# Kernel tuning notes

Measured on AMD Instinct MI355X. Metric: run time of the kernel, lower is better.

Reference implementation:

```python
import jax, jax.numpy as jnp
import numpy as np

N_NODES = 100000
N_EDGES = 1600000
HIDDEN = 128
N_ETYPES = 4
N_STEPS = 4


def setup_inputs() -> dict:
    key = jax.random.key(0)
    ks = jax.random.split(key, 10)
    s = 1.0 / np.sqrt(HIDDEN)
    node_feat = jax.random.normal(ks[0], (N_NODES, HIDDEN), dtype=jnp.float32)
    edge_index = jax.random.randint(ks[1], (2, N_EDGES), 0, N_NODES)
    edge_feat = jax.random.uniform(ks[2], (N_EDGES, N_ETYPES), dtype=jnp.float32)
    # per-edge-type linear layers (DGL GatedGraphConv uses nn.Linear per etype)
    W_edge = jax.random.uniform(ks[3], (N_ETYPES, HIDDEN, HIDDEN), minval=-s, maxval=s, dtype=jnp.float32)
    b_edge = jax.random.uniform(ks[4], (N_ETYPES, HIDDEN), minval=-s, maxval=s, dtype=jnp.float32)
    # GRUCell parameters (torch layout: gates stacked r, z, n)
    W_ih = jax.random.uniform(ks[5], (3 * HIDDEN, HIDDEN), minval=-s, maxval=s, dtype=jnp.float32)
    W_hh = jax.random.uniform(ks[6], (3 * HIDDEN, HIDDEN), minval=-s, maxval=s, dtype=jnp.float32)
    b_ih = jax.random.uniform(ks[7], (3 * HIDDEN,), minval=-s, maxval=s, dtype=jnp.float32)
    b_hh = jax.random.uniform(ks[8], (3 * HIDDEN,), minval=-s, maxval=s, dtype=jnp.float32)
    return {"node_feat": node_feat, "edge_index": edge_index, "edge_feat": edge_feat,
            "W_edge": W_edge, "b_edge": b_edge, "W_ih": W_ih, "W_hh": W_hh,
            "b_ih": b_ih, "b_hh": b_hh}


def _gru_cell(x, h, W_ih, W_hh, b_ih, b_hh):
    gi = x @ W_ih.T + b_ih  # (N, 3D)
    gh = h @ W_hh.T + b_hh
    ir, iz, inn = jnp.split(gi, 3, axis=1)
    hr, hz, hn = jnp.split(gh, 3, axis=1)
    r = jax.nn.sigmoid(ir + hr)
    z = jax.nn.sigmoid(iz + hz)
    n = jnp.tanh(inn + r * hn)
    return (1.0 - z) * n + z * h


def reference(node_feat, edge_index, edge_feat, W_edge, b_edge, W_ih, W_hh, b_ih, b_hh):
    etypes = jnp.argmax(edge_feat, axis=1)          # (E,)
    src, dst = edge_index[0], edge_index[1]
    N = node_feat.shape[0]
    h = node_feat
    for _ in range(N_STEPS):
        # per-etype linear transform of all nodes: (T, N, D)
        trans = jnp.einsum('nd,tod->tno', h, W_edge) + b_edge[:, None, :]
        msg = trans[etypes, src]                    # (E, D) gather by (etype, src)
        a = jax.ops.segment_sum(msg, dst, num_segments=N)  # scatter-add to dst
        h = _gru_cell(a, h, W_ih, W_hh, b_ih, b_hh)
    return h
```

## Files before the change

### kernel.cpp

```cpp
#include <hip/hip_runtime.h>

#define N_NODES 100000
#define N_EDGES 1600000
#define HID 128
#define SCAN_N (N_NODES*4)
#define NB1 ((SCAN_N + 1023) / 1024)
#define ZERO_IDX (N_NODES*4)

#define EB 8192
#define NBLKA ((N_EDGES + EB - 1) / EB)
#define BSH 9
#define NBUCK ((N_NODES + (1<<BSH) - 1) >> BSH)
#define N2 (NBUCK * NBLKA)
#define NB2 ((N2 + 1023) / 1024)

typedef __attribute__((ext_vector_type(8))) short short8;
typedef __attribute__((ext_vector_type(4))) float float4v;
typedef __attribute__((ext_vector_type(4))) int int4v;
typedef __attribute__((ext_vector_type(2))) unsigned int uint2v;
typedef unsigned short ushort_t;
typedef unsigned int uint_t;

__device__ __forceinline__ float bits2f(uint_t u){ union{uint_t u; float f;} x; x.u=u; return x.f; }
__device__ __forceinline__ float b2f(ushort_t u){ return bits2f(((uint_t)u)<<16); }
__device__ __forceinline__ ushort_t f2b(float f){
  union{float f; uint_t u;} x; x.f=f;
  uint_t r = x.u + 0x7fffu + ((x.u>>16)&1u);
  return (ushort_t)(r>>16);
}
__device__ __forceinline__ float sigm(float x){ return 1.0f/(1.0f+__expf(-x)); }
__device__ __forceinline__ float tanh_f(float x){
  float t=__expf(-2.0f*fabsf(x)); float y=(1.0f-t)/(1.0f+t); return x>=0.f? y : -y;
}
__device__ __forceinline__ int imin(int a, int b){ return a < b ? a : b; }


__global__ void prep_weights(const float* __restrict__ W_edge, const float* __restrict__ W_ih,
                             const float* __restrict__ W_hh, ushort_t* __restrict__ WY,
                             ushort_t* __restrict__ W2){
  int i = blockIdx.x*256 + threadIdx.x;
  if (i < 65536){
    WY[i] = f2b(W_edge[i]);
  } else if (i < 65536 + 131072){
    int i2 = i - 65536;
    int n_l = i2 >> 8, k = i2 & 255;
    int wn = n_l >> 7, j = (n_l >> 4) & 7, rr = n_l & 15;
    int c = wn*32 + (j&1)*16 + rr;
    int jg = j >> 1;
    float v;
    if (jg < 2)       v = (k < 128) ? W_ih[(jg*128 + c)*128 + k] : W_hh[(jg*128 + c)*128 + (k-128)];
    else if (jg == 2) v = (k < 128) ? W_ih[(256 + c)*128 + k] : 0.0f;
    else              v = (k >= 128) ? W_hh[(256 + c)*128 + (k-128)] : 0.0f;
    W2[n_l*256 + k] = f2b(v);
  }
}

__global__ void edge_pass1(const int* __restrict__ eidx, const float* __restrict__ efeat,
                           int* __restrict__ packed, int* __restrict__ cnt,
                           int* __restrict__ bcntT){
  __shared__ int hist[NBUCK];
  int tid = threadIdx.x, blk = blockIdx.x;
  for (int j = tid; j < NBUCK; j += 512) hist[j] = 0;
  __syncthreads();
  #pragma unroll
  for (int k = 0; k < EB/512; ++k){
    int e = blk*EB + k*512 + tid;
    if (e < N_EDGES){
      int src = eidx[e], dst = eidx[N_EDGES + e];
      float4v f = *(const float4v*)(efeat + (size_t)e*4);
      int t = 0; float b = f[0];
      if (f[1] > b){ b = f[1]; t = 1; }
      if (f[2] > b){ b = f[2]; t = 2; }
      if (f[3] > b){ b = f[3]; t = 3; }
      packed[e] = (src << 2) | t;
      atomicAdd(&cnt[dst*4 + t], 1);
      atomicAdd(&hist[dst >> BSH], 1);
    }
  }
  __syncthreads();
  for (int j = tid; j < NBUCK; j += 512) bcntT[j*NBLKA + blk] = hist[j];
}

__global__ void scan_pass1(const int* __restrict__ src, int* __restrict__ bsum, int n){
  __shared__ int ws[4];
  int tid = threadIdx.x, lane = tid & 63, w = tid >> 6;
  int idx = blockIdx.x*1024 + tid*4;
  int v = 0;
  if (idx + 3 < n){ int4v x = *(const int4v*)(src + idx); v = x[0]+x[1]+x[2]+x[3]; }
  else { for (int k = 0; k < 4; ++k) if (idx + k < n) v += src[idx+k]; }
  for (int d = 32; d; d >>= 1) v += __shfl_down(v, d);
  if (lane == 0) ws[w] = v;
  __syncthreads();
  if (tid == 0) bsum[blockIdx.x] = ws[0]+ws[1]+ws[2]+ws[3];
}

__global__ void scan_pass2(const int* __restrict__ bsum, int* __restrict__ bpre,
                           int* __restrict__ total_out, int nb){
  __shared__ int sh[512];
  int tid = threadIdx.x;
  int v = (tid < nb) ? bsum[tid] : 0;
  sh[tid] = v;
  __syncthreads();
  for (int d = 1; d < 512; d <<= 1){
    int y = (tid >= d) ? sh[tid-d] : 0;
    __syncthreads();
    sh[tid] += y;
    __syncthreads();
  }
  if (tid < nb) bpre[tid] = sh[tid] - v;
  if (tid == 511) *total_out = sh[511];
}

__global__ void scan_pass3(const int* __restrict__ src, const int* __restrict__ bpre,
                           int* __restrict__ off, int n){
  __shared__ int wsum[4];
  int tid = threadIdx.x, lane = tid & 63, w = tid >> 6;
  int idx = blockIdx.x*1024 + tid*4;
  int v0=0,v1=0,v2=0,v3=0;
  if (idx + 3 < n){ int4v x = *(const int4v*)(src + idx); v0=x[0];v1=x[1];v2=x[2];v3=x[3]; }
  else {
    if (idx   < n) v0 = src[idx];
    if (idx+1 < n) v1 = src[idx+1];
    if (idx+2 < n) v2 = src[idx+2];
    if (idx+3 < n) v3 = src[idx+3];
  }
  int ts = v0+v1+v2+v3;
  int sc = ts;
  for (int d = 1; d < 64; d <<= 1){ int y = __shfl_up(sc, d); if (lane >= d) sc += y; }
  if (lane == 63) wsum[w] = sc;
  __syncthreads();
  int wofs = 0;
  for (int k = 0; k < w; ++k) wofs += wsum[k];
  int base = bpre[blockIdx.x] + wofs + sc - ts;
  int e0 = base, e1 = e0+v0, e2 = e1+v1, e3 = e2+v2;
  if (idx   < n) off[idx  ] = e0;
  if (idx+1 < n) off[idx+1] = e1;
  if (idx+2 < n) off[idx+2] = e2;
  if (idx+3 < n) off[idx+3] = e3;
}

__global__ void bucket_scatter(const int* __restrict__ eidx, const int* __restrict__ packed,
                               const int* __restrict__ boffT, int* __restrict__ bucketed){
  __shared__ int cur[NBUCK];
  int tid = threadIdx.x, blk = blockIdx.x;
  for (int j = tid; j < NBUCK; j += 512) cur[j] = boffT[j*NBLKA + blk];
  __syncthreads();
  #pragma unroll
  for (int k = 0; k < EB/512; ++k){
    int e = blk*EB + k*512 + tid;
    if (e < N_EDGES){
      int dst = eidx[N_EDGES + e];
      int pos = atomicAdd(&cur[dst >> BSH], 1);
      bucketed[pos] = ((dst & ((1<<BSH)-1)) << 19) | packed[e];
    }
  }
}

__global__ void bucket_sort(const int* __restrict__ bucketed, const int* __restrict__ boffT,
                            const int* __restrict__ off4, int* __restrict__ sorted){
  __shared__ int cur[(1<<BSH)*4];
  int tid = threadIdx.x, b = blockIdx.x;
  int base = b * ((1<<BSH)*4);
  for (int j = tid; j < (1<<BSH)*4; j += 512)
    cur[j] = off4[imin(base + j, SCAN_N)];
  __syncthreads();
  int s = boffT[b*NBLKA];
  int e = boffT[(b+1)*NBLKA];
  for (int i = s + tid; i < e; i += 512){
    int w = bucketed[i];
    int ci = ((w >> 19) << 2) | (w & 3);
    int pos = atomicAdd(&cur[ci], 1);
    sorted[pos] = w & 0x7FFFF;
  }
}

__global__ void init_h(const float* __restrict__ nf, ushort_t* __restrict__ hB, int n4){
  int i = blockIdx.x*256 + threadIdx.x;
  if (i >= n4) return;
  float4v v = *(const float4v*)(nf + (size_t)i*4);
  uint2v u;
  u[0] = (uint_t)f2b(v[0]) | ((uint_t)f2b(v[1])<<16);
  u[1] = (uint_t)f2b(v[2]) | ((uint_t)f2b(v[3])<<16);
  *(uint2v*)(hB + (size_t)i*4) = u;
}


__launch_bounds__(512, 2)
__global__ void transform_kernel(const ushort_t* __restrict__ hB, const ushort_t* __restrict__ WY,
                                 ushort_t* __restrict__ Y){
  __shared__ ushort_t lA[128*64];
  __shared__ ushort_t lB[512*64];
  int tid = threadIdx.x, w = tid >> 6, lane = tid & 63;
  int wm = w >> 2, wn = w & 3;
  int row0 = blockIdx.x * 128;
  float4v acc[4][8] = {};
  for (int kt = 0; kt < 2; ++kt){
    short8 va[2], vb[8];
    #pragma unroll
    for (int i = 0; i < 2; ++i){
      int cidx = i*512 + tid;
      int r = cidx >> 3, ch = cidx & 7;
      int node = row0 + r; if (node >= N_NODES) node = N_NODES-1;
      va[i] = *reinterpret_cast<const short8*>(hB + (size_t)node*128 + kt*64 + ch*8);
    }
    #pragma unroll
    for (int i = 0; i < 8; ++i){
      int cidx = i*512 + tid;
      int n = cidx >> 3, ch = cidx & 7;
      vb[i] = *reinterpret_cast<const short8*>(WY + (size_t)n*128 + kt*64 + ch*8);
    }
    __syncthreads();
    #pragma unroll
    for (int i = 0; i < 2; ++i){
      int cidx = i*512 + tid;
      int r = cidx >> 3, ch = cidx & 7;
      *reinterpret_cast<short8*>(lA + r*64 + ((ch ^ (r&7))<<3)) = va[i];
    }
    #pragma unroll
    for (int i = 0; i < 8; ++i){
      int cidx = i*512 + tid;
      int n = cidx >> 3, ch = cidx & 7;
      *reinterpret_cast<short8*>(lB + n*64 + ((ch ^ (n&7))<<3)) = vb[i];
    }
    __syncthreads();
    #pragma unroll
    for (int kk = 0; kk < 2; ++kk){
      int lch = kk*4 + (lane>>4);
      short8 af[4], bf[8];
      #pragma unroll
      for (int i = 0; i < 4; ++i){
        int r = wm*64 + i*16 + (lane&15);
        af[i] = *reinterpret_cast<const short8*>(lA + r*64 + ((lch ^ (r&7))<<3));
      }
      #pragma unroll
      for (int j = 0; j < 8; ++j){
        int n = wn*128 + j*16 + (lane&15);
        bf[j] = *reinterpret_cast<const short8*>(lB + n*64 + ((lch ^ (n&7))<<3));
      }
      #pragma unroll
      for (int i = 0; i < 4; ++i)
        #pragma unroll
        for (int j = 0; j < 8; ++j)
          acc[i][j] = __builtin_amdgcn_mfma_f32_16x16x32_bf16(af[i], bf[j], acc[i][j], 0, 0, 0);
    }
    __syncthreads();
  }
  #pragma unroll
  for (int i = 0; i < 4; ++i)
    #pragma unroll
    for (int j = 0; j < 8; ++j)
      #pragma unroll
      for (int q = 0; q < 4; ++q){
        int grow = row0 + wm*64 + i*16 + (lane>>4)*4 + q;
        if (grow >= N_NODES) continue;
        int colc = wn*128 + j*16 + (lane&15);
        Y[(size_t)grow*512 + colc] = f2b(acc[i][j][q]);
      }
}

__global__ void agg_kernel(const int* __restrict__ off4, const int* __restrict__ sorted,
                           const ushort_t* __restrict__ Y, const int* __restrict__ cnt,
                           const float* __restrict__ b_edge, ushort_t* __restrict__ aB){
  int wid = (int)((blockIdx.x * blockDim.x + threadIdx.x) >> 6);
  int lane = threadIdx.x & 63;
  if (wid >= N_NODES) return;
  int s = off4[wid*4], e = off4[wid*4+4];
  int col = lane*2;
  float p0=0,p1=0,q0=0,q1=0,r0=0,r1=0,t0=0,t1=0;
  for (int i = s; i < e; i += 16){
    int vv[16];
    #pragma unroll
    for (int k = 0; k < 16; ++k){
      int j = i + k;
      int sv = sorted[imin(j, e-1)];
      vv[k] = __builtin_amdgcn_readfirstlane(j < e ? sv : ZERO_IDX);
    }
    uint_t hv[16];
    #pragma unroll
    for (int k = 0; k < 16; ++k)
      hv[k] = *(const uint_t*)(Y + (size_t)vv[k]*128 + col);
    #pragma unroll
    for (int k = 0; k < 16; ++k){
      float f0 = bits2f((hv[k] & 0xffffu) << 16);
      float f1 = bits2f(hv[k] & 0xffff0000u);
      if ((k&3)==0){ p0+=f0; p1+=f1; }
      else if ((k&3)==1){ q0+=f0; q1+=f1; }
      else if ((k&3)==2){ r0+=f0; r1+=f1; }
      else { t0+=f0; t1+=f1; }
    }
  }
  float s0 = (p0+q0)+(r0+t0);
  float s1 = (p1+q1)+(r1+t1);
  int4v c4 = *(const int4v*)(cnt + wid*4);
  #pragma unroll
  for (int t = 0; t < 4; ++t){
    float cf = (float)c4[t];
    s0 += cf * b_edge[t*128 + col];
    s1 += cf * b_edge[t*128 + col + 1];
  }
  *(uint_t*)(aB + (size_t)wid*128 + col) = (uint_t)f2b(s0) | ((uint_t)f2b(s1) << 16);
}

__launch_bounds__(512, 2)
__global__ void gru_tr_kernel(const ushort_t* __restrict__ aB, ushort_t* __restrict__ hB,
                              const ushort_t* __restrict__ W2, const ushort_t* __restrict__ WY,
                              const float* __restrict__ b_ih, const float* __restrict__ b_hh,
                              float* __restrict__ hF, ushort_t* __restrict__ Y, int last){
  __shared__ ushort_t lA[128*64];
  __shared__ ushort_t lB[512*64];
  int tid = threadIdx.x, w = tid >> 6, lane = tid & 63;
  int wm = w >> 2, wn = w & 3;
  int l15 = lane & 15, lq = lane >> 4;
  int row0 = blockIdx.x * 128;
  {
    float4v acc[4][8] = {};
    for (int kt = 0; kt < 4; ++kt){
      short8 va[2], vb[8];
      const ushort_t* srcA = (kt < 2) ? aB : hB;
      #pragma unroll
      for (int i = 0; i < 2; ++i){
        int cidx = i*512 + tid;
        int r = cidx >> 3, ch = cidx & 7;
        int node = row0 + r; if (node >= N_NODES) node = N_NODES-1;
        va[i] = *reinterpret_cast<const short8*>(srcA + (size_t)node*128 + (kt&1)*64 + ch*8);
      }
      #pragma unroll
      for (int i = 0; i < 8; ++i){
        int cidx = i*512 + tid;
        int n = cidx >> 3, ch = cidx & 7;
        vb[i] = *reinterpret_cast<const short8*>(W2 + (size_t)n*256 + kt*64 + ch*8);
      }
      __syncthreads();
      #pragma unroll
      for (int i = 0; i < 2; ++i){
        int cidx = i*512 + tid;
        int r = cidx >> 3, ch = cidx & 7;
        *reinterpret_cast<short8*>(lA + r*64 + ((ch ^ (r&7))<<3)) = va[i];
      }
      #pragma unroll
      for (int i = 0; i < 8; ++i){
        int cidx = i*512 + tid;
        int n = cidx >> 3, ch = cidx & 7;
        *reinterpret_cast<short8*>(lB + n*64 + ((ch ^ (n&7))<<3)) = vb[i];
      }
      __syncthreads();
      bool lo = (kt < 2);
      #pragma unroll
      for (int kk = 0; kk < 2; ++kk){
        int lch = kk*4 + lq;
        short8 af[4], bf[8];
        #pragma unroll
        for (int i = 0; i < 4; ++i){
          int r = wm*64 + i*16 + l15;
          af[i] = *reinterpret_cast<const short8*>(lA + r*64 + ((lch ^ (r&7))<<3));
        }
        #pragma unroll
        for (int j = 0; j < 8; ++j){
          if (lo ? (j >= 6) : (j == 4 || j == 5)) continue;
          int n = wn*128 + j*16 + l15;
          bf[j] = *reinterpret_cast<const short8*>(lB + n*64 + ((lch ^ (n&7))<<3));
          #pragma unroll
          for (int i = 0; i < 4; ++i)
            acc[i][j] = __builtin_amdgcn_mfma_f32_16x16x32_bf16(af[i], bf[j], acc[i][j], 0, 0, 0);
        }
      }
      __syncthreads();
    }
    #pragma unroll
    for (int i = 0; i < 4; ++i){
      #pragma unroll
      for (int jj = 0; jj < 2; ++jj){
        int c = wn*32 + jj*16 + l15;
        float bir = b_ih[c] + b_hh[c];
        float biz = b_ih[128+c] + b_hh[128+c];
        float bni = b_ih[256+c], bnh = b_hh[256+c];
        int ch = c >> 3;
        #pragma unroll
        for (int q = 0; q < 4; ++q){
          int row = wm*64 + i*16 + lq*4 + q;
          int grow = row0 + row;
          float rg = sigm(acc[i][0+jj][q] + bir);
          float zg = sigm(acc[i][2+jj][q] + biz);
          float hn = acc[i][6+jj][q] + bnh;
          float nn = tanh_f(acc[i][4+jj][q] + bni + rg*hn);
          int rc = imin(grow, N_NODES-1);
          float h = b2f(hB[(size_t)rc*128 + c]);
          float out = (1.0f - zg)*nn + zg*h;
          ushort_t ob = f2b(out);
          lB[16384 + row*128 + ((ch ^ (row&15))<<3) + (c&7)] = ob;
          if (grow < N_NODES){
            hB[(size_t)grow*128 + c] = ob;
            if (last) hF[(size_t)grow*128 + c] = out;
          }
        }
      }
    }
  }
  if (last) return;
  __syncthreads();
  #pragma unroll
  for (int nh = 0; nh < 2; ++nh){
    float4v acc2[4][4] = {};
    #pragma unroll
    for (int kt = 0; kt < 2; ++kt){
      short8 vw[4];
      #pragma unroll
      for (int i = 0; i < 4; ++i){
        int cidx = i*512 + tid;
        int n = cidx >> 3, ch = cidx & 7;
        vw[i] = *reinterpret_cast<const short8*>(WY + (size_t)(nh*256 + n)*128 + kt*64 + ch*8);
      }
      __syncthreads();
      #pragma unroll
      for (int i = 0; i < 4; ++i){
        int cidx = i*512 + tid;
        int n = cidx >> 3, ch = cidx & 7;
        *reinterpret_cast<short8*>(lB + n*64 + ((ch ^ (n&7))<<3)) = vw[i];
      }
      __syncthreads();
      #pragma unroll
      for (int kk = 0; kk < 2; ++kk){
        int lchh = kt*8 + kk*4 + lq;
        int lchw = kk*4 + lq;
        short8 af[4], bf[4];
        #pragma unroll
        for (int i = 0; i < 4; ++i){
          int r = wm*64 + i*16 + l15;
          af[i] = *reinterpret_cast<const short8*>(lB + 16384 + r*128 + ((lchh ^ (r&15))<<3));
        }
        #pragma unroll
        for (int j = 0; j < 4; ++j){
          int n = wn*64 + j*16 + l15;
          bf[j] = *reinterpret_cast<const short8*>(lB + n*64 + ((lchw ^ (n&7))<<3));
        }
        #pragma unroll
        for (int i = 0; i < 4; ++i)
          #pragma unroll
          for (int j = 0; j < 4; ++j)
            acc2[i][j] = __builtin_amdgcn_mfma_f32_16x16x32_bf16(af[i], bf[j], acc2[i][j], 0, 0, 0);
      }
    }
    #pragma unroll
    for (int i = 0; i < 4; ++i)
      #pragma unroll
      for (int q = 0; q < 4; ++q){
        int grow = row0 + wm*64 + i*16 + lq*4 + q;
        if (grow >= N_NODES) continue;
        #pragma unroll
        for (int j = 0; j < 4; ++j)
          Y[(size_t)grow*512 + nh*256 + wn*64 + j*16 + l15] = f2b(acc2[i][j][q]);
      }
  }
}


extern "C" void kernel_launch(void* const* d_in, const int* in_sizes, int n_in,
                              void* d_out, int out_size, void* d_ws, size_t ws_size,
                              hipStream_t stream) {
  const float* node_feat = (const float*)d_in[0];
  const int*   edge_idx  = (const int*)d_in[1];
  const float* edge_feat = (const float*)d_in[2];
  const float* W_edge    = (const float*)d_in[3];
  const float* b_edge    = (const float*)d_in[4];
  const float* W_ih      = (const float*)d_in[5];
  const float* W_hh      = (const float*)d_in[6];
  const float* b_ih      = (const float*)d_in[7];
  const float* b_hh      = (const float*)d_in[8];
  float* hF = (float*)d_out;

  char* p = (char*)d_ws;
  auto take = [&](size_t bytes) -> char* {
    char* r = p; p += (bytes + 255) & ~(size_t)255; return r;
  };
  ushort_t* WY     = (ushort_t*)take(512*128*2);
  ushort_t* W2     = (ushort_t*)take(512*256*2);
  int* cnt      = (int*)take((size_t)SCAN_N*4);
  int* off4     = (int*)take((size_t)(SCAN_N+1)*4);
  int* bcntT    = (int*)take((size_t)N2*4);
  int* boffT    = (int*)take((size_t)(N2+1)*4);
  int* bsum     = (int*)take(512*4);
  int* bpre     = (int*)take(512*4);
  int* packed   = (int*)take((size_t)N_EDGES*4);
  int* bucketed = (int*)take((size_t)N_EDGES*4);
  int* sorted   = (int*)take((size_t)N_EDGES*4);
  ushort_t* hB = (ushort_t*)take((size_t)N_NODES*128*2);
  ushort_t* Y  = (ushort_t*)take(((size_t)N_NODES*512 + 256)*2);
  ushort_t* aB = (ushort_t*)take((size_t)N_NODES*128*2);

  hipMemsetAsync(cnt, 0, (size_t)SCAN_N*4, stream);
  hipMemsetAsync(Y + (size_t)N_NODES*512, 0, 256*2, stream);

  prep_weights<<<768, 256, 0, stream>>>(W_edge, W_ih, W_hh, WY, W2);
  edge_pass1<<<NBLKA, 512, 0, stream>>>(edge_idx, edge_feat, packed, cnt, bcntT);
  scan_pass1<<<NB1, 256, 0, stream>>>(cnt, bsum, SCAN_N);
  scan_pass2<<<1, 512, 0, stream>>>(bsum, bpre, off4 + SCAN_N, NB1);
  scan_pass3<<<NB1, 256, 0, stream>>>(cnt, bpre, off4, SCAN_N);
  scan_pass1<<<NB2, 256, 0, stream>>>(bcntT, bsum, N2);
  scan_pass2<<<1, 512, 0, stream>>>(bsum, bpre, boffT + N2, NB2);
  scan_pass3<<<NB2, 256, 0, stream>>>(bcntT, bpre, boffT, N2);
  bucket_scatter<<<NBLKA, 512, 0, stream>>>(edge_idx, packed, boffT, bucketed);
  bucket_sort<<<NBUCK, 512, 0, stream>>>(bucketed, boffT, off4, sorted);
  init_h<<<(N_NODES*32 + 255)/256, 256, 0, stream>>>(node_feat, hB, N_NODES*32);

  int gb = (N_NODES + 127) / 128;
  transform_kernel<<<gb, 512, 0, stream>>>(hB, WY, Y);
  for (int step = 0; step < 4; ++step){
    agg_kernel<<<(N_NODES+3)/4, 256, 0, stream>>>(off4, sorted, Y, cnt, b_edge, aB);
    gru_tr_kernel<<<gb, 512, 0, stream>>>(aB, hB, W2, WY, b_ih, b_hh, hF, Y, step == 3);
  }
}
```

Before: 805.9 us.

## Load MFMA weight fragments directly from pre-swizzled global layout, double-buffer activations

Weights for the GRU and transform GEMMs are pre-permuted into per-lane MFMA fragment order, so each wave reads B operands straight from global/L2 instead of staging them through LDS. Activation tiles are double-buffered in LDS with next-tile prefetch, which cuts barriers per k-step, and the GRU reads h from the staged LDS tile rather than global memory. LDS use drops, which may allow higher occupancy, at the cost of repeated global weight reads per wave that rely on cache hits.

```diff
diff --git a/kernel.cpp b/kernel.cpp
--- a/kernel.cpp
+++ b/kernel.cpp
@@ -37,21 +37,33 @@
 
 __global__ void prep_weights(const float* __restrict__ W_edge, const float* __restrict__ W_ih,
                              const float* __restrict__ W_hh, ushort_t* __restrict__ WY,
-                             ushort_t* __restrict__ W2){
+                             ushort_t* __restrict__ W2f, ushort_t* __restrict__ WYf){
   int i = blockIdx.x*256 + threadIdx.x;
   if (i < 65536){
     WY[i] = f2b(W_edge[i]);
   } else if (i < 65536 + 131072){
     int i2 = i - 65536;
-    int n_l = i2 >> 8, k = i2 & 255;
-    int wn = n_l >> 7, j = (n_l >> 4) & 7, rr = n_l & 15;
-    int c = wn*32 + (j&1)*16 + rr;
+    int tile = i2 >> 9, e9 = i2 & 511;
+    int lane = e9 >> 3, e = e9 & 7;
+    int kk = tile & 1, kt = (tile >> 1) & 3, j = (tile >> 3) & 7, wn = tile >> 6;
+    int lq = lane >> 4, l15 = lane & 15;
+    int c = wn*32 + (j&1)*16 + l15;
     int jg = j >> 1;
+    int k = kt*64 + (kk*4 + lq)*8 + e;
     float v;
     if (jg < 2)       v = (k < 128) ? W_ih[(jg*128 + c)*128 + k] : W_hh[(jg*128 + c)*128 + (k-128)];
     else if (jg == 2) v = (k < 128) ? W_ih[(256 + c)*128 + k] : 0.0f;
     else              v = (k >= 128) ? W_hh[(256 + c)*128 + (k-128)] : 0.0f;
-    W2[n_l*256 + k] = f2b(v);
+    W2f[i2] = f2b(v);
+  } else if (i < 65536 + 131072 + 65536){
+    int i3 = i - 65536 - 131072;
+    int tile = i3 >> 9, e9 = i3 & 511;
+    int lane = e9 >> 3, e = e9 & 7;
+    int kc = tile & 3, j = (tile >> 2) & 3, wn = (tile >> 4) & 3, nh = tile >> 6;
+    int lq = lane >> 4, l15 = lane & 15;
+    int n = nh*256 + wn*64 + j*16 + l15;
+    int k = kc*32 + lq*8 + e;
+    WYf[i3] = f2b(W_edge[n*128 + k]);
   }
 }
 
@@ -303,95 +315,96 @@
 
 __launch_bounds__(512, 2)
 __global__ void gru_tr_kernel(const ushort_t* __restrict__ aB, ushort_t* __restrict__ hB,
-                              const ushort_t* __restrict__ W2, const ushort_t* __restrict__ WY,
+                              const ushort_t* __restrict__ W2f, const ushort_t* __restrict__ WYf,
                               const float* __restrict__ b_ih, const float* __restrict__ b_hh,
                               float* __restrict__ hF, ushort_t* __restrict__ Y, int last){
-  __shared__ ushort_t lA[128*64];
-  __shared__ ushort_t lB[512*64];
+  __shared__ ushort_t lA[2][8192];
+  __shared__ ushort_t lH[16384];
   int tid = threadIdx.x, w = tid >> 6, lane = tid & 63;
   int wm = w >> 2, wn = w & 3;
   int l15 = lane & 15, lq = lane >> 4;
   int row0 = blockIdx.x * 128;
+
+  int cidx0 = tid, r0l = cidx0 >> 3, ch0 = cidx0 & 7;
+  int cidx1 = 512 + tid, r1l = cidx1 >> 3, ch1 = cidx1 & 7;
+  int node0 = imin(row0 + r0l, N_NODES-1);
+  int node1 = imin(row0 + r1l, N_NODES-1);
+  size_t aoff0 = (size_t)node0*128 + ch0*8;
+  size_t aoff1 = (size_t)node1*128 + ch1*8;
+  int wo0 = r0l*64 + ((ch0 ^ (r0l&7))<<3);
+  int wo1 = r1l*64 + ((ch1 ^ (r1l&7))<<3);
+
   {
-    float4v acc[4][8] = {};
-    for (int kt = 0; kt < 4; ++kt){
-      short8 va[2], vb[8];
-      const ushort_t* srcA = (kt < 2) ? aB : hB;
-      #pragma unroll
-      for (int i = 0; i < 2; ++i){
-        int cidx = i*512 + tid;
-        int r = cidx >> 3, ch = cidx & 7;
-        int node = row0 + r; if (node >= N_NODES) node = N_NODES-1;
-        va[i] = *reinterpret_cast<const short8*>(srcA + (size_t)node*128 + (kt&1)*64 + ch*8);
-      }
-      #pragma unroll
-      for (int i = 0; i < 8; ++i){
-        int cidx = i*512 + tid;
-        int n = cidx >> 3, ch = cidx & 7;
-        vb[i] = *reinterpret_cast<const short8*>(W2 + (size_t)n*256 + kt*64 + ch*8);
-      }
-      __syncthreads();
-      #pragma unroll
-      for (int i = 0; i < 2; ++i){
-        int cidx = i*512 + tid;
-        int r = cidx >> 3, ch = cidx & 7;
-        *reinterpret_cast<short8*>(lA + r*64 + ((ch ^ (r&7))<<3)) = va[i];
-      }
-      #pragma unroll
-      for (int i = 0; i < 8; ++i){
-        int cidx = i*512 + tid;
-        int n = cidx >> 3, ch = cidx & 7;
-        *reinterpret_cast<short8*>(lB + n*64 + ((ch ^ (n&7))<<3)) = vb[i];
-      }
-      __syncthreads();
-      bool lo = (kt < 2);
-      #pragma unroll
-      for (int kk = 0; kk < 2; ++kk){
-        int lch = kk*4 + lq;
-        short8 af[4], bf[8];
+    short8 va0 = *reinterpret_cast<const short8*>(aB + aoff0);
+    short8 va1 = *reinterpret_cast<const short8*>(aB + aoff1);
+    *reinterpret_cast<short8*>(&lA[0][wo0]) = va0;
+    *reinterpret_cast<short8*>(&lA[0][wo1]) = va1;
+  }
+  __syncthreads();
+
+  float4v acc[4][8] = {};
+  #pragma unroll
+  for (int kt = 0; kt < 4; ++kt){
+    short8 vn0, vn1;
+    if (kt < 3){
+      const ushort_t* srcN = (kt+1 < 2) ? aB : hB;
+      int koff = ((kt+1)&1)*64;
+      vn0 = *reinterpret_cast<const short8*>(srcN + aoff0 + koff);
+      vn1 = *reinterpret_cast<const short8*>(srcN + aoff1 + koff);
+    }
+    bool lo = (kt < 2);
+    const ushort_t* lcur = lA[kt&1];
+    #pragma unroll
+    for (int kk = 0; kk < 2; ++kk){
+      int lch = kk*4 + lq;
+      short8 af[4];
+      #pragma unroll
+      for (int i = 0; i < 4; ++i){
+        int r = wm*64 + i*16 + l15;
+        af[i] = *reinterpret_cast<const short8*>(lcur + r*64 + ((lch ^ (r&7))<<3));
+      }
+      #pragma unroll
+      for (int j = 0; j < 8; ++j){
+        if (lo ? (j >= 6) : (j == 4 || j == 5)) continue;
+        int tile = ((wn*8 + j)*4 + kt)*2 + kk;
+        short8 bf = *reinterpret_cast<const short8*>(W2f + (size_t)tile*512 + lane*8);
         #pragma unroll
-        for (int i = 0; i < 4; ++i){
-          int r = wm*64 + i*16 + l15;
-          af[i] = *reinterpret_cast<const short8*>(lA + r*64 + ((lch ^ (r&7))<<3));
-        }
-        #pragma unroll
-        for (int j = 0; j < 8; ++j){
-          if (lo ? (j >= 6) : (j == 4 || j == 5)) continue;
-          int n = wn*128 + j*16 + l15;
-          bf[j] = *reinterpret_cast<const short8*>(lB + n*64 + ((lch ^ (n&7))<<3));
-          #pragma unroll
-          for (int i = 0; i < 4; ++i)
-            acc[i][j] = __builtin_amdgcn_mfma_f32_16x16x32_bf16(af[i], bf[j], acc[i][j], 0, 0, 0);
-        }
-      }
-      __syncthreads();
-    }
-    #pragma unroll
-    for (int i = 0; i < 4; ++i){
-      #pragma unroll
-      for (int jj = 0; jj < 2; ++jj){
-        int c = wn*32 + jj*16 + l15;
-        float bir = b_ih[c] + b_hh[c];
-        float biz = b_ih[128+c] + b_hh[128+c];
-        float bni = b_ih[256+c], bnh = b_hh[256+c];
-        int ch = c >> 3;
-        #pragma unroll
-        for (int q = 0; q < 4; ++q){
-          int row = wm*64 + i*16 + lq*4 + q;
-          int grow = row0 + row;
-          float rg = sigm(acc[i][0+jj][q] + bir);
-          float zg = sigm(acc[i][2+jj][q] + biz);
-          float hn = acc[i][6+jj][q] + bnh;
-          float nn = tanh_f(acc[i][4+jj][q] + bni + rg*hn);
-          int rc = imin(grow, N_NODES-1);
-          float h = b2f(hB[(size_t)rc*128 + c]);
-          float out = (1.0f - zg)*nn + zg*h;
-          ushort_t ob = f2b(out);
-          lB[16384 + row*128 + ((ch ^ (row&15))<<3) + (c&7)] = ob;
-          if (grow < N_NODES){
-            hB[(size_t)grow*128 + c] = ob;
-            if (last) hF[(size_t)grow*128 + c] = out;
-          }
+        for (int i = 0; i < 4; ++i)
+          acc[i][j] = __builtin_amdgcn_mfma_f32_16x16x32_bf16(af[i], bf, acc[i][j], 0, 0, 0);
+      }
+    }
+    if (kt < 3){
+      *reinterpret_cast<short8*>(&lA[(kt+1)&1][wo0]) = vn0;
+      *reinterpret_cast<short8*>(&lA[(kt+1)&1][wo1]) = vn1;
+    }
+    __syncthreads();
+  }
+  #pragma unroll
+  for (int i = 0; i < 4; ++i){
+    #pragma unroll
+    for (int jj = 0; jj < 2; ++jj){
+      int c = wn*32 + jj*16 + l15;
+      float bir = b_ih[c] + b_hh[c];
+      float biz = b_ih[128+c] + b_hh[128+c];
+      float bni = b_ih[256+c], bnh = b_hh[256+c];
+      int cl = c & 63;
+      const ushort_t* lh = lA[c >> 6];
+      int ch = c >> 3;
+      #pragma unroll
+      for (int q = 0; q < 4; ++q){
+        int row = wm*64 + i*16 + lq*4 + q;
+        int grow = row0 + row;
+        float rg = sigm(acc[i][0+jj][q] + bir);
+        float zg = sigm(acc[i][2+jj][q] + biz);
+        float hn = acc[i][6+jj][q] + bnh;
+        float nn = tanh_f(acc[i][4+jj][q] + bni + rg*hn);
+        float h = b2f(lh[row*64 + (((cl>>3) ^ (row&7))<<3) + (cl&7)]);
+        float out = (1.0f - zg)*nn + zg*h;
+        ushort_t ob = f2b(out);
+        lH[row*128 + ((ch ^ (row&15))<<3) + (c&7)] = ob;
+        if (grow < N_NODES){
+          hB[(size_t)grow*128 + c] = ob;
+          if (last) hF[(size_t)grow*128 + c] = out;
         }
       }
     }
@@ -402,42 +415,21 @@
   for (int nh = 0; nh < 2; ++nh){
     float4v acc2[4][4] = {};
     #pragma unroll
-    for (int kt = 0; kt < 2; ++kt){
-      short8 vw[4];
+    for (int kc = 0; kc < 4; ++kc){
+      int lchh = kc*4 + lq;
+      short8 af[4];
       #pragma unroll
       for (int i = 0; i < 4; ++i){
-        int cidx = i*512 + tid;
-        int n = cidx >> 3, ch = cidx & 7;
-        vw[i] = *reinterpret_cast<const short8*>(WY + (size_t)(nh*256 + n)*128 + kt*64 + ch*8);
-      }
-      __syncthreads();
-      #pragma unroll
-      for (int i = 0; i < 4; ++i){
-        int cidx = i*512 + tid;
-        int n = cidx >> 3, ch = cidx & 7;
-        *reinterpret_cast<short8*>(lB + n*64 + ((ch ^ (n&7))<<3)) = vw[i];
-      }
-      __syncthreads();
-      #pragma unroll
-      for (int kk = 0; kk < 2; ++kk){
-        int lchh = kt*8 + kk*4 + lq;
-        int lchw = kk*4 + lq;
-        short8 af[4], bf[4];
-        #pragma unroll
-        for (int i = 0; i < 4; ++i){
-          int r = wm*64 + i*16 + l15;
-          af[i] = *reinterpret_cast<const short8*>(lB + 16384 + r*128 + ((lchh ^ (r&15))<<3));
-        }
-        #pragma unroll
-        for (int j = 0; j < 4; ++j){
-          int n = wn*64 + j*16 + l15;
-          bf[j] = *reinterpret_cast<const short8*>(lB + n*64 + ((lchw ^ (n&7))<<3));
-        }
+        int r = wm*64 + i*16 + l15;
+        af[i] = *reinterpret_cast<const short8*>(lH + r*128 + ((lchh ^ (r&15))<<3));
+      }
+      #pragma unroll
+      for (int j = 0; j < 4; ++j){
+        int tile = ((nh*4 + wn)*4 + j)*4 + kc;
+        short8 bf = *reinterpret_cast<const short8*>(WYf + (size_t)tile*512 + lane*8);
         #pragma unroll
         for (int i = 0; i < 4; ++i)
-          #pragma unroll
-          for (int j = 0; j < 4; ++j)
-            acc2[i][j] = __builtin_amdgcn_mfma_f32_16x16x32_bf16(af[i], bf[j], acc2[i][j], 0, 0, 0);
+          acc2[i][j] = __builtin_amdgcn_mfma_f32_16x16x32_bf16(af[i], bf, acc2[i][j], 0, 0, 0);
       }
     }
     #pragma unroll
@@ -473,7 +465,8 @@
     char* r = p; p += (bytes + 255) & ~(size_t)255; return r;
   };
   ushort_t* WY     = (ushort_t*)take(512*128*2);
-  ushort_t* W2     = (ushort_t*)take(512*256*2);
+  ushort_t* W2f    = (ushort_t*)take(131072*2);
+  ushort_t* WYf    = (ushort_t*)take(65536*2);
   int* cnt      = (int*)take((size_t)SCAN_N*4);
   int* off4     = (int*)take((size_t)(SCAN_N+1)*4);
   int* bcntT    = (int*)take((size_t)N2*4);
@@ -490,7 +483,7 @@
   hipMemsetAsync(cnt, 0, (size_t)SCAN_N*4, stream);
   hipMemsetAsync(Y + (size_t)N_NODES*512, 0, 256*2, stream);
 
-  prep_weights<<<768, 256, 0, stream>>>(W_edge, W_ih, W_hh, WY, W2);
+  prep_weights<<<1024, 256, 0, stream>>>(W_edge, W_ih, W_hh, WY, W2f, WYf);
   edge_pass1<<<NBLKA, 512, 0, stream>>>(edge_idx, edge_feat, packed, cnt, bcntT);
   scan_pass1<<<NB1, 256, 0, stream>>>(cnt, bsum, SCAN_N);
   scan_pass2<<<1, 512, 0, stream>>>(bsum, bpre, off4 + SCAN_N, NB1);
@@ -506,6 +499,6 @@
   transform_kernel<<<gb, 512, 0, stream>>>(hB, WY, Y);
   for (int step = 0; step < 4; ++step){
     agg_kernel<<<(N_NODES+3)/4, 256, 0, stream>>>(off4, sorted, Y, cnt, b_edge, aB);
-    gru_tr_kernel<<<gb, 512, 0, stream>>>(aB, hB, W2, WY, b_ih, b_hh, hF, Y, step == 3);
-  }
-}
+    gru_tr_kernel<<<gb, 512, 0, stream>>>(aB, hB, W2f, WYf, b_ih, b_hh, hF, Y, step == 3);
+  }
+}
```

Result: no change. 815.0 us (+1.1%).
